# Performance work log

Measured on AMD Instinct MI355X. Metric: run time of the kernel, lower is better.

## Reference

```python
import jax, jax.numpy as jnp
import numpy as np

HEAD_QK_SIZE = 256
VOCAB_SIZE = 32000


def setup_inputs() -> dict:
    key = jax.random.key(0)
    k1, k2, k3, k4 = jax.random.split(key, 4)
    T, C, D = 4096, 1024, HEAD_QK_SIZE
    x = jax.random.normal(k1, (T, C), dtype=jnp.float32)
    idx = jax.random.randint(k2, (T,), 0, VOCAB_SIZE, dtype=jnp.int64)
    # Dense kernels (no bias), scaled like default lecun init magnitude
    Wq = jax.random.normal(k3, (C, D), dtype=jnp.float32) / np.sqrt(C)
    Wk = jax.random.normal(k4, (C, D), dtype=jnp.float32) / np.sqrt(C)
    return {"x": x, "idx": idx, "Wq": Wq, "Wk": Wk}


def reference(x, idx, Wq, Wk):
    # x: [T, C], idx: [T]
    T = x.shape[0]
    q = x @ Wq  # [T, D]
    k = x @ Wk  # [T, D]
    c = (q @ k.T) * (1.0 / HEAD_QK_SIZE)  # [T, T]
    causal = jnp.tril(jnp.ones((T, T), dtype=bool))
    c = jnp.where(causal, c, jnp.zeros((), dtype=c.dtype))
    # c @ one_hot(idx, vocab) == scatter-add of c's columns into vocab slots
    out = jax.ops.segment_sum(c.T, idx, num_segments=VOCAB_SIZE).T  # [T, vocab]
    return out
```

## Files before the change

### kernel.cpp

```cpp
#include <hip/hip_runtime.h>
#include <math.h>

constexpr int T = 4096;
constexpr int C = 1024;
constexpr int D = 256;
constexpr int VOCAB = 32000;
constexpr int VQ = VOCAB / 4;
constexpr int NT = T / 64;
constexpr int NTILES = NT * (NT + 1) / 2;

typedef __attribute__((ext_vector_type(8))) short bf16x8;
typedef __attribute__((ext_vector_type(4))) float f32x4;

__device__ inline unsigned short f2bf(float f) {
    union { float f; unsigned int u; } v; v.f = f;
    unsigned int u = v.u + 0x7FFFu + ((v.u >> 16) & 1u);
    return (unsigned short)(u >> 16);
}
__device__ inline float bf2f(unsigned short s) {
    union { unsigned int u; float f; } v; v.u = ((unsigned int)s) << 16;
    return v.f;
}
__device__ inline void gl_lds16(const unsigned short* g, unsigned short* l) {
    __builtin_amdgcn_global_load_lds(
        (const __attribute__((address_space(1))) unsigned int*)g,
        (__attribute__((address_space(3))) unsigned int*)l, 16, 0, 0);
}

__global__ __launch_bounds__(256) void prep_kernel(
    const float* __restrict__ x,
    const float* __restrict__ Wq, const float* __restrict__ Wk,
    unsigned short* __restrict__ xb, unsigned short* __restrict__ WT)
{
    const int tid = threadIdx.x;
    if (blockIdx.x < 2048) {
        const int i = (blockIdx.x * 256 + tid) * 8;
        float4 a = *(const float4*)(x + i);
        float4 b = *(const float4*)(x + i + 4);
        union { bf16x8 v; unsigned short s[8]; } o;
        o.s[0] = f2bf(a.x); o.s[1] = f2bf(a.y); o.s[2] = f2bf(a.z); o.s[3] = f2bf(a.w);
        o.s[4] = f2bf(b.x); o.s[5] = f2bf(b.y); o.s[6] = f2bf(b.z); o.s[7] = f2bf(b.w);
        *(bf16x8*)(xb + i) = o.v;
    } else {
        const int bid = blockIdx.x - 2048;
        const int w  = bid >> 6;
        const int rem = bid & 63;
        const int k0 = (rem >> 2) * 64;
        const int n0 = (rem & 3) * 64;
        const float* W = w ? Wk : Wq;
        __shared__ float tile[64][65];
        #pragma unroll
        for (int p = 0; p < 16; ++p) {
            const int e = p * 256 + tid;
            const int r = e >> 6, c = e & 63;
            tile[c][r] = W[(size_t)(k0 + r) * D + n0 + c];
        }
        __syncthreads();
        #pragma unroll
        for (int p = 0; p < 2; ++p) {
            const int e = p * 256 + tid;
            const int rr = e >> 3, cc = e & 7;
            union { bf16x8 v; unsigned short s[8]; } o;
            #pragma unroll
            for (int i = 0; i < 8; ++i) o.s[i] = f2bf(tile[rr][cc * 8 + i]);
            *(bf16x8*)(WT + (size_t)(w * D + n0 + rr) * C + k0 + cc * 8) = o.v;
        }
    }
}

__global__ __launch_bounds__(256) void qk_mfma_kernel(
    const unsigned short* __restrict__ xb,
    const unsigned short* __restrict__ WT,
    unsigned short* __restrict__ qk)
{
    const int m0 = blockIdx.x * 64, n0 = blockIdx.y * 64;
    __shared__ __align__(16) unsigned short As[64 * 64];
    __shared__ __align__(16) unsigned short Bs[64 * 64];
    const int tid = threadIdx.x;
    const int wave = tid >> 6, lane = tid & 63;
    const int quad = lane >> 4, lr = lane & 15;
    const int wm = wave >> 1, wn = wave & 1;
    const int rsub = lane >> 3, c8 = (lane & 7) * 8;

    f32x4 acc[2][2] = {};

    for (int k0 = 0; k0 < C; k0 += 64) {
        #pragma unroll
        for (int q = 0; q < 2; ++q) {
            const int ch = wave * 2 + q;
            const int r = ch * 8 + rsub;
            gl_lds16(xb + (size_t)(m0 + r) * C + k0 + c8, As + ch * 512);
            gl_lds16(WT + (size_t)(n0 + r) * C + k0 + c8, Bs + ch * 512);
        }
        __syncthreads();
        #pragma unroll
        for (int kk = 0; kk < 64; kk += 32) {
            bf16x8 a[2], b[2];
            #pragma unroll
            for (int s = 0; s < 2; ++s) {
                a[s] = *(const bf16x8*)(As + (wm * 32 + s * 16 + lr) * 64 + kk + quad * 8);
                b[s] = *(const bf16x8*)(Bs + (wn * 32 + s * 16 + lr) * 64 + kk + quad * 8);
            }
            #pragma unroll
            for (int i = 0; i < 2; ++i)
                #pragma unroll
                for (int j = 0; j < 2; ++j)
                    acc[i][j] = __builtin_amdgcn_mfma_f32_16x16x32_bf16(
                        a[i], b[j], acc[i][j], 0, 0, 0);
        }
        __syncthreads();
    }

    #pragma unroll
    for (int i = 0; i < 2; ++i)
        #pragma unroll
        for (int j = 0; j < 2; ++j)
            #pragma unroll
            for (int r = 0; r < 4; ++r) {
                const int row = m0 + wm * 32 + i * 16 + quad * 4 + r;
                const int col = n0 + wn * 32 + j * 16 + lr;
                qk[(size_t)row * 512 + col] = f2bf(acc[i][j][r]);
            }
}

__global__ __launch_bounds__(256) void qkt_mfma_kernel(
    const unsigned short* __restrict__ qk,
    unsigned short* __restrict__ cpack)
{
    const int bid = blockIdx.x;
    int ti = (int)((sqrtf(8.0f * (float)bid + 1.0f) - 1.0f) * 0.5f);
    while ((ti + 1) * (ti + 2) / 2 <= bid) ++ti;
    while (ti * (ti + 1) / 2 > bid) --ti;
    const int tj = bid - ti * (ti + 1) / 2;

    __shared__ __align__(16) unsigned short As[64 * 64];
    __shared__ __align__(16) unsigned short Bs[64 * 64];
    const int tid = threadIdx.x;
    const int wave = tid >> 6, lane = tid & 63;
    const int quad = lane >> 4, lr = lane & 15;
    const int wm = wave >> 1, wn = wave & 1;
    const int rsub = lane >> 3, c8 = (lane & 7) * 8;

    f32x4 acc[2][2] = {};

    const unsigned short* qp = qk + (size_t)ti * 64 * 512;
    const unsigned short* kp = qk + (size_t)tj * 64 * 512 + 256;

    for (int k0 = 0; k0 < D; k0 += 64) {
        #pragma unroll
        for (int q = 0; q < 2; ++q) {
            const int ch = wave * 2 + q;
            const int r = ch * 8 + rsub;
            gl_lds16(qp + (size_t)r * 512 + k0 + c8, As + ch * 512);
            gl_lds16(kp + (size_t)r * 512 + k0 + c8, Bs + ch * 512);
        }
        __syncthreads();
        #pragma unroll
        for (int kk = 0; kk < 64; kk += 32) {
            bf16x8 a[2], b[2];
            #pragma unroll
            for (int s = 0; s < 2; ++s) {
                a[s] = *(const bf16x8*)(As + (wm * 32 + s * 16 + lr) * 64 + kk + quad * 8);
                b[s] = *(const bf16x8*)(Bs + (wn * 32 + s * 16 + lr) * 64 + kk + quad * 8);
            }
            #pragma unroll
            for (int i = 0; i < 2; ++i)
                #pragma unroll
                for (int j = 0; j < 2; ++j)
                    acc[i][j] = __builtin_amdgcn_mfma_f32_16x16x32_bf16(
                        a[i], b[j], acc[i][j], 0, 0, 0);
        }
        __syncthreads();
    }

    const float scale = 1.0f / 256.0f;
    unsigned short* Cs = As;
    #pragma unroll
    for (int i = 0; i < 2; ++i)
        #pragma unroll
        for (int j = 0; j < 2; ++j)
            #pragma unroll
            for (int r = 0; r < 4; ++r) {
                const int row = wm * 32 + i * 16 + quad * 4 + r;
                const int col = wn * 32 + j * 16 + lr;
                const int rg = ti * 64 + row, cg = tj * 64 + col;
                Cs[row * 64 + col] = f2bf((cg <= rg) ? acc[i][j][r] * scale : 0.0f);
            }
    __syncthreads();

    const size_t tbase = (size_t)4096 * ((size_t)ti * (ti + 1) / 2);
    const int len = (ti + 1) * 64;
    #pragma unroll
    for (int p = 0; p < 2; ++p) {
        const int cidx = p * 256 + tid;
        const int row = cidx >> 3, o8 = (cidx & 7) * 8;
        *(bf16x8*)(cpack + tbase + (size_t)row * len + tj * 64 + o8) =
            *(const bf16x8*)(Cs + row * 64 + o8);
    }
}

__global__ __launch_bounds__(256) void row_scatter_kernel(
    const unsigned short* __restrict__ cpack,
    const int* __restrict__ idx,
    float* __restrict__ out)
{
    __shared__ f32x4 hist4[VQ / 4];
    float* hist = (float*)hist4;

    const int t  = blockIdx.x;
    const int lo = blockIdx.y * VQ;
    const int tid = threadIdx.x;

    const f32x4 z4 = {0.0f, 0.0f, 0.0f, 0.0f};
    for (int v = tid; v < VQ / 4; v += 256) hist4[v] = z4;
    __syncthreads();

    const int ti = t >> 6, il = t & 63;
    const int len = (ti + 1) * 64;
    const unsigned short* rowp =
        cpack + (size_t)4096 * ((size_t)ti * (ti + 1) / 2) + (size_t)il * len;
    const int nch = len >> 3;

    for (int ch = tid; ch < nch; ch += 256) {
        union { bf16x8 v; unsigned short s[8]; } cv;
        cv.v = *(const bf16x8*)(rowp + ch * 8);
        union { int4 a[2]; int j[8]; } ji;
        ji.a[0] = *(const int4*)(idx + ch * 8);
        ji.a[1] = *(const int4*)(idx + ch * 8 + 4);
        #pragma unroll
        for (int i = 0; i < 8; ++i) {
            const int v = ji.j[i] - lo;
            if ((unsigned)v < (unsigned)VQ) {
                const float f = bf2f(cv.s[i]);
                if (f != 0.0f) atomicAdd(&hist[v], f);
            }
        }
    }
    __syncthreads();

    f32x4* orow = (f32x4*)(out + (size_t)t * VOCAB + lo);
    for (int v = tid; v < VQ / 4; v += 256)
        __builtin_nontemporal_store(hist4[v], orow + v);
}

extern "C" void kernel_launch(void* const* d_in, const int* in_sizes, int n_in,
                              void* d_out, int out_size, void* d_ws, size_t ws_size,
                              hipStream_t stream)
{
    const float* x   = (const float*)d_in[0];
    const int*   idx = (const int*)d_in[1];
    const float* Wq  = (const float*)d_in[2];
    const float* Wk  = (const float*)d_in[3];
    float* out = (float*)d_out;

    unsigned short* xb = (unsigned short*)d_ws;
    unsigned short* WT = xb + (size_t)T * C;
    unsigned short* qk = WT + (size_t)2 * D * C;
    unsigned short* cpack = qk + (size_t)T * 2 * D;

    prep_kernel<<<dim3(2048 + 128), 256, 0, stream>>>(x, Wq, Wk, xb, WT);
    qk_mfma_kernel<<<dim3(T / 64, (2 * D) / 64), 256, 0, stream>>>(xb, WT, qk);
    qkt_mfma_kernel<<<dim3(NTILES), 256, 0, stream>>>(qk, cpack);
    row_scatter_kernel<<<dim3(T, 4), 256, 0, stream>>>(cpack, idx, out);
}
```

Before: 564.2 us.

## Fuse QK^T with vocab scatter via bucketed token lists per vocab tile

Replaces the packed causal score matrix and row-wise LDS histogram scatter with a single kernel tiled over (64 query rows, 64-wide vocab tile). A new single-block bucket kernel groups key positions by vocab tile. Each block gathers the key rows that map into its tile, computes their scores with MFMA, and accumulates them into a small LDS output tile that is stored directly. This removes the intermediate bf16 score matrix write and read and the large per-row histograms. In exchange it recomputes scores per vocab tile using gathered rows, runs many blocks with tiny or empty key lists, and adds a serial one-block bucketing pass.

```diff
diff --git a/kernel.cpp b/kernel.cpp
--- a/kernel.cpp
+++ b/kernel.cpp
@@ -1,13 +1,12 @@
 #include <hip/hip_runtime.h>
-#include <math.h>
 
 constexpr int T = 4096;
 constexpr int C = 1024;
 constexpr int D = 256;
 constexpr int VOCAB = 32000;
-constexpr int VQ = VOCAB / 4;
-constexpr int NT = T / 64;
-constexpr int NTILES = NT * (NT + 1) / 2;
+constexpr int VT = 64;
+constexpr int NVT = VOCAB / VT;
+constexpr int SENT = 0x7FFFFFFF;
 
 typedef __attribute__((ext_vector_type(8))) short bf16x8;
 typedef __attribute__((ext_vector_type(4))) float f32x4;
@@ -16,10 +15,6 @@
     union { float f; unsigned int u; } v; v.f = f;
     unsigned int u = v.u + 0x7FFFu + ((v.u >> 16) & 1u);
     return (unsigned short)(u >> 16);
-}
-__device__ inline float bf2f(unsigned short s) {
-    union { unsigned int u; float f; } v; v.u = ((unsigned int)s) << 16;
-    return v.f;
 }
 __device__ inline void gl_lds16(const unsigned short* g, unsigned short* l) {
     __builtin_amdgcn_global_load_lds(
@@ -68,6 +63,33 @@
     }
 }
 
+__global__ __launch_bounds__(256) void bucket_kernel(
+    const int* __restrict__ idx, int* __restrict__ offs, int* __restrict__ lists)
+{
+    __shared__ int cnt[NVT];
+    __shared__ int base_s[NVT];
+    const int tid = threadIdx.x;
+    for (int v = tid; v < NVT; v += 256) cnt[v] = 0;
+    __syncthreads();
+    for (int j = tid; j < T; j += 256) atomicAdd(&cnt[idx[j] / VT], 1);
+    __syncthreads();
+    if (tid == 0) {
+        int run = 0;
+        for (int v = 0; v < NVT; ++v) { base_s[v] = run; run += cnt[v]; }
+    }
+    __syncthreads();
+    for (int v = tid; v < NVT; v += 256) offs[v] = base_s[v];
+    if (tid == 0) offs[NVT] = T;
+    __syncthreads();
+    for (int v = tid; v < NVT; v += 256) cnt[v] = 0;
+    __syncthreads();
+    for (int j = tid; j < T; j += 256) {
+        const int v = idx[j] / VT;
+        const int pos = atomicAdd(&cnt[v], 1);
+        lists[base_s[v] + pos] = (j << 6) | (idx[j] & (VT - 1));
+    }
+}
+
 __global__ __launch_bounds__(256) void qk_mfma_kernel(
     const unsigned short* __restrict__ xb,
     const unsigned short* __restrict__ WT,
@@ -123,124 +145,77 @@
             }
 }
 
-__global__ __launch_bounds__(256) void qkt_mfma_kernel(
+__global__ __launch_bounds__(256) void scatter_mfma_kernel(
     const unsigned short* __restrict__ qk,
-    unsigned short* __restrict__ cpack)
-{
-    const int bid = blockIdx.x;
-    int ti = (int)((sqrtf(8.0f * (float)bid + 1.0f) - 1.0f) * 0.5f);
-    while ((ti + 1) * (ti + 2) / 2 <= bid) ++ti;
-    while (ti * (ti + 1) / 2 > bid) --ti;
-    const int tj = bid - ti * (ti + 1) / 2;
-
-    __shared__ __align__(16) unsigned short As[64 * 64];
-    __shared__ __align__(16) unsigned short Bs[64 * 64];
+    const int* __restrict__ offs,
+    const int* __restrict__ lists,
+    float* __restrict__ out)
+{
+    __shared__ __align__(16) unsigned short As[64 * 256];
+    __shared__ __align__(16) unsigned short Bs[16 * 256];
+    __shared__ __align__(16) float Ot[64 * VT];
+    __shared__ int jent[16];
+
+    const int ti = blockIdx.x;
+    const int vt = blockIdx.y;
     const int tid = threadIdx.x;
     const int wave = tid >> 6, lane = tid & 63;
     const int quad = lane >> 4, lr = lane & 15;
-    const int wm = wave >> 1, wn = wave & 1;
-    const int rsub = lane >> 3, c8 = (lane & 7) * 8;
-
-    f32x4 acc[2][2] = {};
-
-    const unsigned short* qp = qk + (size_t)ti * 64 * 512;
-    const unsigned short* kp = qk + (size_t)tj * 64 * 512 + 256;
-
-    for (int k0 = 0; k0 < D; k0 += 64) {
-        #pragma unroll
-        for (int q = 0; q < 2; ++q) {
-            const int ch = wave * 2 + q;
-            const int r = ch * 8 + rsub;
-            gl_lds16(qp + (size_t)r * 512 + k0 + c8, As + ch * 512);
-            gl_lds16(kp + (size_t)r * 512 + k0 + c8, Bs + ch * 512);
-        }
-        __syncthreads();
-        #pragma unroll
-        for (int kk = 0; kk < 64; kk += 32) {
-            bf16x8 a[2], b[2];
-            #pragma unroll
-            for (int s = 0; s < 2; ++s) {
-                a[s] = *(const bf16x8*)(As + (wm * 32 + s * 16 + lr) * 64 + kk + quad * 8);
-                b[s] = *(const bf16x8*)(Bs + (wn * 32 + s * 16 + lr) * 64 + kk + quad * 8);
-            }
-            #pragma unroll
-            for (int i = 0; i < 2; ++i)
-                #pragma unroll
-                for (int j = 0; j < 2; ++j)
-                    acc[i][j] = __builtin_amdgcn_mfma_f32_16x16x32_bf16(
-                        a[i], b[j], acc[i][j], 0, 0, 0);
-        }
-        __syncthreads();
-    }
-
+
+    const unsigned short* qbase = qk + (size_t)ti * 64 * 512;
+    #pragma unroll
+    for (int p = 0; p < 8; ++p) {
+        const int r = p * 8 + wave * 2 + (lane >> 5);
+        gl_lds16(qbase + (size_t)r * 512 + (lane & 31) * 8,
+                 As + (p * 8 + wave * 2) * 256);
+    }
+    f32x4* Ot4 = (f32x4*)Ot;
+    const f32x4 z4 = {0.0f, 0.0f, 0.0f, 0.0f};
+    #pragma unroll
+    for (int i = 0; i < 4; ++i) Ot4[i * 256 + tid] = z4;
+
+    const int off0 = offs[vt], off1 = offs[vt + 1];
     const float scale = 1.0f / 256.0f;
-    unsigned short* Cs = As;
-    #pragma unroll
-    for (int i = 0; i < 2; ++i)
-        #pragma unroll
-        for (int j = 0; j < 2; ++j)
-            #pragma unroll
-            for (int r = 0; r < 4; ++r) {
-                const int row = wm * 32 + i * 16 + quad * 4 + r;
-                const int col = wn * 32 + j * 16 + lr;
-                const int rg = ti * 64 + row, cg = tj * 64 + col;
-                Cs[row * 64 + col] = f2bf((cg <= rg) ? acc[i][j][r] * scale : 0.0f);
-            }
-    __syncthreads();
-
-    const size_t tbase = (size_t)4096 * ((size_t)ti * (ti + 1) / 2);
-    const int len = (ti + 1) * 64;
-    #pragma unroll
-    for (int p = 0; p < 2; ++p) {
-        const int cidx = p * 256 + tid;
-        const int row = cidx >> 3, o8 = (cidx & 7) * 8;
-        *(bf16x8*)(cpack + tbase + (size_t)row * len + tj * 64 + o8) =
-            *(const bf16x8*)(Cs + row * 64 + o8);
-    }
-}
-
-__global__ __launch_bounds__(256) void row_scatter_kernel(
-    const unsigned short* __restrict__ cpack,
-    const int* __restrict__ idx,
-    float* __restrict__ out)
-{
-    __shared__ f32x4 hist4[VQ / 4];
-    float* hist = (float*)hist4;
-
-    const int t  = blockIdx.x;
-    const int lo = blockIdx.y * VQ;
-    const int tid = threadIdx.x;
-
-    const f32x4 z4 = {0.0f, 0.0f, 0.0f, 0.0f};
-    for (int v = tid; v < VQ / 4; v += 256) hist4[v] = z4;
-    __syncthreads();
-
-    const int ti = t >> 6, il = t & 63;
-    const int len = (ti + 1) * 64;
-    const unsigned short* rowp =
-        cpack + (size_t)4096 * ((size_t)ti * (ti + 1) / 2) + (size_t)il * len;
-    const int nch = len >> 3;
-
-    for (int ch = tid; ch < nch; ch += 256) {
-        union { bf16x8 v; unsigned short s[8]; } cv;
-        cv.v = *(const bf16x8*)(rowp + ch * 8);
-        union { int4 a[2]; int j[8]; } ji;
-        ji.a[0] = *(const int4*)(idx + ch * 8);
-        ji.a[1] = *(const int4*)(idx + ch * 8 + 4);
-        #pragma unroll
-        for (int i = 0; i < 8; ++i) {
-            const int v = ji.j[i] - lo;
-            if ((unsigned)v < (unsigned)VQ) {
-                const float f = bf2f(cv.s[i]);
-                if (f != 0.0f) atomicAdd(&hist[v], f);
-            }
-        }
-    }
-    __syncthreads();
-
-    f32x4* orow = (f32x4*)(out + (size_t)t * VOCAB + lo);
-    for (int v = tid; v < VQ / 4; v += 256)
-        __builtin_nontemporal_store(hist4[v], orow + v);
+
+    for (int g = off0; g < off1; g += 16) {
+        if (tid < 16) jent[tid] = (g + tid < off1) ? lists[g + tid] : SENT;
+        __syncthreads();
+        #pragma unroll
+        for (int p = 0; p < 2; ++p) {
+            const int rl = p * 8 + wave * 2 + (lane >> 5);
+            int j = jent[rl] >> 6; if (j > T - 1) j = 0;
+            gl_lds16(qk + (size_t)j * 512 + 256 + (lane & 31) * 8,
+                     Bs + (p * 8 + wave * 2) * 256);
+        }
+        __syncthreads();
+
+        f32x4 acc = {0.0f, 0.0f, 0.0f, 0.0f};
+        #pragma unroll
+        for (int k0 = 0; k0 < 256; k0 += 32) {
+            bf16x8 a = *(const bf16x8*)(As + (wave * 16 + lr) * 256 + k0 + quad * 8);
+            bf16x8 b = *(const bf16x8*)(Bs + lr * 256 + k0 + quad * 8);
+            acc = __builtin_amdgcn_mfma_f32_16x16x32_bf16(a, b, acc, 0, 0, 0);
+        }
+        const int e = jent[lr];
+        const int j = e >> 6, lc = e & (VT - 1);
+        #pragma unroll
+        for (int r = 0; r < 4; ++r) {
+            const int rloc = wave * 16 + quad * 4 + r;
+            const int t = ti * 64 + rloc;
+            if (j <= t) atomicAdd(&Ot[rloc * VT + lc], acc[r] * scale);
+        }
+        __syncthreads();
+    }
+    __syncthreads();
+
+    float* obase = out + (size_t)ti * 64 * VOCAB + (size_t)vt * VT;
+    #pragma unroll
+    for (int i = 0; i < 4; ++i) {
+        const int q4 = i * 256 + tid;
+        const int rloc = q4 >> 4, c4 = q4 & 15;
+        __builtin_nontemporal_store(Ot4[q4],
+            (f32x4*)(obase + (size_t)rloc * VOCAB + c4 * 4));
+    }
 }
 
 extern "C" void kernel_launch(void* const* d_in, const int* in_sizes, int n_in,
@@ -256,10 +231,11 @@
     unsigned short* xb = (unsigned short*)d_ws;
     unsigned short* WT = xb + (size_t)T * C;
     unsigned short* qk = WT + (size_t)2 * D * C;
-    unsigned short* cpack = qk + (size_t)T * 2 * D;
+    int* lists = (int*)(qk + (size_t)T * 2 * D);
+    int* offs  = lists + T;
 
     prep_kernel<<<dim3(2048 + 128), 256, 0, stream>>>(x, Wq, Wk, xb, WT);
+    bucket_kernel<<<dim3(1), 256, 0, stream>>>(idx, offs, lists);
     qk_mfma_kernel<<<dim3(T / 64, (2 * D) / 64), 256, 0, stream>>>(xb, WT, qk);
-    qkt_mfma_kernel<<<dim3(NTILES), 256, 0, stream>>>(qk, cpack);
-    row_scatter_kernel<<<dim3(T, 4), 256, 0, stream>>>(cpack, idx, out);
-}
+    scatter_mfma_kernel<<<dim3(T / 64, NVT), 256, 0, stream>>>(qk, offs, lists, out);
+}
```

Result: slower. 702.3 us (+24.5%).
